# Kernel tuning notes

Measured on AMD Instinct MI355X. Metric: run time of the kernel, lower is better.

The kernel has to match this reference:

```python
import jax, jax.numpy as jnp
import numpy as np

COMMITMENT_COST = 0.25
EPS = 1e-12  # F.normalize default eps


def _l2_normalize(x):
    n = jnp.linalg.norm(x, axis=-1, keepdims=True)
    return x / jnp.maximum(n, EPS)


def setup_inputs() -> dict:
    key = jax.random.key(0)
    k1, k2 = jax.random.split(key)
    inputs = jax.random.normal(k1, (32, 1024, 256), dtype=jnp.float32)
    codebooks = jax.random.normal(k2, (8, 1024, 256), dtype=jnp.float32)
    return {"inputs": inputs, "codebooks": codebooks}


def reference(inputs, codebooks):
    # inputs: (B, T, D); codebooks: (Q, C, D)
    Q, C, D = codebooks.shape
    sg = jax.lax.stop_gradient
    residual = inputs
    quantized_sum = jnp.zeros_like(inputs)
    losses = []
    idx_list = []
    for qi in range(Q):
        cb = codebooks[qi]                              # (C, D)
        flat = residual.reshape(-1, D)                  # (N, D)
        sim = jnp.matmul(_l2_normalize(flat), _l2_normalize(cb).T)  # (N, C)
        indices = jnp.argmax(sim, axis=1)               # argmin(1 - sim) == argmax(sim)
        q = cb[indices].reshape(residual.shape)         # (B, T, D)
        e_latent = jnp.mean((sg(q) - residual) ** 2)
        q_latent = jnp.mean((q - sg(residual)) ** 2)
        losses.append(q_latent + COMMITMENT_COST * e_latent)
        q_st = residual + sg(q - residual)              # straight-through
        quantized_sum = quantized_sum + q_st
        residual = residual - q_st
        idx_list.append(indices)
    total_vq_loss = jnp.mean(jnp.stack(losses))
    indices_all = jnp.stack(idx_list)[..., None]        # (Q, N, 1) int32
    return (quantized_sum, total_vq_loss, indices_all)
```

## Files before the change

### kernel.cpp

```cpp
#include <hip/hip_runtime.h>
#include <math.h>

#define QN 8
#define CN 1024
#define DN 256
#define NROWS 32768

#define LOSS_OFF 8388608
#define IDX_OFF  8388609

typedef float f32x4v __attribute__((ext_vector_type(4)));
typedef short v8s __attribute__((ext_vector_type(8)));
typedef unsigned short u16;
typedef unsigned short u16x8 __attribute__((ext_vector_type(8)));

__device__ __forceinline__ u16 bfr(float x) {
    unsigned u = __float_as_uint(x);
    u += 0x7FFFu + ((u >> 16) & 1u);
    return (u16)(u >> 16);
}
__device__ __forceinline__ float bfs(u16 h) { return __uint_as_float(((unsigned)h) << 16); }

__device__ __forceinline__ void acpB(u16* d, const u16* s) {
    __builtin_amdgcn_global_load_lds(
        (const __attribute__((address_space(1))) unsigned int*)s,
        (__attribute__((address_space(3))) unsigned int*)d, 16, 0, 0);
}

__global__ void rvq_prep(const float* __restrict__ cb,
                         u16* __restrict__ bh, u16* __restrict__ bm,
                         float* __restrict__ invw,
                         float* __restrict__ out) {
    if (blockIdx.x == 0 && threadIdx.x == 0) out[LOSS_OFF] = 0.0f;
    const int wave = threadIdx.x >> 6;
    const int lane = threadIdx.x & 63;
    const int cw = blockIdx.x * 4 + wave;
    float4 v = reinterpret_cast<const float4*>(cb + (size_t)cw * DN)[lane];
    float ss = v.x * v.x + v.y * v.y + v.z * v.z + v.w * v.w;
#pragma unroll
    for (int m = 1; m < 64; m <<= 1) ss += __shfl_xor(ss, m, 64);
    const float inv = 1.0f / fmaxf(sqrtf(ss), 1e-12f);
    if (lane == 0) invw[cw] = inv;
    ushort4 hv, mv;
#define PSPLIT(F, E) { const float x_ = (F) * inv; const u16 h_ = bfr(x_); \
                       hv.E = h_; mv.E = bfr(x_ - bfs(h_)); }
    PSPLIT(v.x, x) PSPLIT(v.y, y) PSPLIT(v.z, z) PSPLIT(v.w, w)
#undef PSPLIT
    reinterpret_cast<ushort4*>(bh + (size_t)cw * DN)[lane] = hv;
    reinterpret_cast<ushort4*>(bm + (size_t)cw * DN)[lane] = mv;
}

__global__ __attribute__((amdgpu_flat_work_group_size(256, 256), amdgpu_waves_per_eu(2, 2)))
void rvq_main(const float* __restrict__ in,
              const float* __restrict__ cb,
              const u16* __restrict__ bh, const u16* __restrict__ bm,
              const float* __restrict__ invw,
              float* __restrict__ out) {
    __shared__ __align__(16) char lds[81920];
    u16* Ah = (u16*)lds;
    u16* Am = (u16*)(lds + 32768);
    u16* Bt = (u16*)(lds + 65536);
    float* Rres = (float*)lds;
    int*   cand = (int*)(lds + 65536);
    int*   sIdx = (int*)(lds + 65536 + 1024);
    float* red  = (float*)(lds + 65536 + 1024 + 256);

    const int t   = threadIdx.x;
    const int l   = t & 63;
    const int w   = t >> 6;
    const int g   = l >> 4;
    const int li  = l & 15;
    const int row = l;
    const int KS  = w * 64;
    const int w8  = w * 8;
    const int w16 = w * 16;
    const int w16li = w16 + li;
    const int base  = blockIdx.x * 64;

    const float* inr0 = in + (size_t)(base + row) * DN + KS;
#define DECLR(i) float4 rr##i = *reinterpret_cast<const float4*>(inr0 + (i) * 4);
    DECLR(0) DECLR(1) DECLR(2) DECLR(3) DECLR(4) DECLR(5) DECLR(6) DECLR(7)
    DECLR(8) DECLR(9) DECLR(10) DECLR(11) DECLR(12) DECLR(13) DECLR(14) DECLR(15)
#undef DECLR
    float lossAcc = 0.0f;

    for (int qs = 0; qs < QN; ++qs) {
        const u16* bhq = bh + ((size_t)qs << 18);
        const u16* bmq = bm + ((size_t)qs << 18);

#define SCV(e, x) { const float xv_ = (x); const u16 hb_ = bfr(xv_); \
                    hh_[e] = hb_; mm_[e] = bfr(xv_ - bfs(hb_)); }
#define SPLITP(p, RA, RB) { u16x8 hh_, mm_; \
        SCV(0, RA.x) SCV(1, RA.y) SCV(2, RA.z) SCV(3, RA.w) \
        SCV(4, RB.x) SCV(5, RB.y) SCV(6, RB.z) SCV(7, RB.w) \
        const int ao_ = ((w8 + (p)) * 64 + row) * 8; \
        *(u16x8*)(Ah + ao_) = hh_; *(u16x8*)(Am + ao_) = mm_; }
        SPLITP(0, rr0, rr1)   SPLITP(1, rr2, rr3)   SPLITP(2, rr4, rr5)
        SPLITP(3, rr6, rr7)   SPLITP(4, rr8, rr9)   SPLITP(5, rr10, rr11)
        SPLITP(6, rr12, rr13) SPLITP(7, rr14, rr15)
#undef SPLITP
#undef SCV

#define STAGE(nb, sp_) { \
        _Pragma("unroll") \
        for (int jj_ = 0; jj_ < 2; ++jj_) { \
            const int d_ = jj_ * 256 + t; \
            const int sub_ = d_ >> 8, pl_ = (d_ >> 7) & 1, kb_ = (d_ >> 5) & 3, col_ = d_ & 31; \
            const int s2_ = (sp_) * 2 + sub_; const int cs2_ = s2_ >> 3, ks2_ = s2_ & 7; \
            const u16* gp_ = (pl_ ? bmq : bhq) + (size_t)(cs2_ * 32 + col_) * DN + ks2_ * 32 + kb_ * 8; \
            acpB(Bt + (nb) * 4096 + d_ * 8, gp_); } }

#define DECLT(j) float v1_##j = -INFINITY, v2_##j = -INFINITY, \
                       v3_##j = -INFINITY, v4_##j = -INFINITY; \
                 int i1_##j = 0, i2_##j = 0, i3_##j = 0, i4_##j = 0;
        DECLT(0) DECLT(1) DECLT(2) DECLT(3)
#undef DECLT
        f32x4v accA = (f32x4v){0.f, 0.f, 0.f, 0.f};
        f32x4v accB = (f32x4v){0.f, 0.f, 0.f, 0.f};

#define MRG4(j, vv, ci) { const float v_ = (vv); const int c_ = (ci); \
        if (v_ > v4_##j) { \
            if (v_ > v2_##j) { \
                if (v_ > v1_##j) { v4_##j = v3_##j; i4_##j = i3_##j; v3_##j = v2_##j; i3_##j = i2_##j; \
                                   v2_##j = v1_##j; i2_##j = i1_##j; v1_##j = v_; i1_##j = c_; } \
                else             { v4_##j = v3_##j; i4_##j = i3_##j; v3_##j = v2_##j; i3_##j = i2_##j; \
                                   v2_##j = v_; i2_##j = c_; } \
            } else { \
                if (v_ > v3_##j) { v4_##j = v3_##j; i4_##j = i3_##j; v3_##j = v_; i3_##j = c_; } \
                else             { v4_##j = v_; i4_##j = c_; } \
            } } }

#define COMPUTE(bb, sub) { \
        const int s_ = sp * 2 + (sub); const int cs_ = s_ >> 3, ks_ = s_ & 7; \
        const int ao_ = ((ks_ * 4 + g) * 64 + w16li) * 8; \
        const v8s ah_ = *(const v8s*)(Ah + ao_); \
        const v8s am_ = *(const v8s*)(Am + ao_); \
        const u16* bt_ = Bt + ((bb) * 2 + (sub)) * 2048; \
        const v8s bh0_ = *(const v8s*)(bt_ + g * 256 + li * 8); \
        const v8s bh1_ = *(const v8s*)(bt_ + g * 256 + 128 + li * 8); \
        const v8s bm0_ = *(const v8s*)(bt_ + 1024 + g * 256 + li * 8); \
        const v8s bm1_ = *(const v8s*)(bt_ + 1024 + g * 256 + 128 + li * 8); \
        accA = __builtin_amdgcn_mfma_f32_16x16x32_bf16(ah_, bh0_, accA, 0, 0, 0); \
        accA = __builtin_amdgcn_mfma_f32_16x16x32_bf16(ah_, bm0_, accA, 0, 0, 0); \
        accA = __builtin_amdgcn_mfma_f32_16x16x32_bf16(am_, bh0_, accA, 0, 0, 0); \
        accA = __builtin_amdgcn_mfma_f32_16x16x32_bf16(am_, bm0_, accA, 0, 0, 0); \
        accB = __builtin_amdgcn_mfma_f32_16x16x32_bf16(ah_, bh1_, accB, 0, 0, 0); \
        accB = __builtin_amdgcn_mfma_f32_16x16x32_bf16(ah_, bm1_, accB, 0, 0, 0); \
        accB = __builtin_amdgcn_mfma_f32_16x16x32_bf16(am_, bh1_, accB, 0, 0, 0); \
        accB = __builtin_amdgcn_mfma_f32_16x16x32_bf16(am_, bm1_, accB, 0, 0, 0); \
        if (ks_ == 7) { \
            const int cb0_ = cs_ * 32 + li; \
            MRG4(0, accA.x, cb0_) MRG4(1, accA.y, cb0_) MRG4(2, accA.z, cb0_) MRG4(3, accA.w, cb0_) \
            MRG4(0, accB.x, cb0_ + 16) MRG4(1, accB.y, cb0_ + 16) \
            MRG4(2, accB.z, cb0_ + 16) MRG4(3, accB.w, cb0_ + 16) \
            accA = (f32x4v){0.f, 0.f, 0.f, 0.f}; accB = (f32x4v){0.f, 0.f, 0.f, 0.f}; } }

        STAGE(0, 0)
        for (int sp = 0; sp < 128; ++sp) {
            __syncthreads();
            const int bb = sp & 1;
            if (sp < 127) STAGE(bb ^ 1, sp + 1)
            COMPUTE(bb, 0)
            COMPUTE(bb, 1)
        }
#undef COMPUTE
#undef STAGE

#define EXT1(j, GD) { \
        const float cv_ = (p_ == 0) ? v1_##j : (p_ == 1) ? v2_##j : \
                          (p_ == 2) ? v3_##j : (p_ == 3) ? v4_##j : -INFINITY; \
        const int   ci_ = (p_ == 0) ? i1_##j : (p_ == 1) ? i2_##j : \
                          (p_ == 2) ? i3_##j : i4_##j; \
        float bv_ = cv_; int bi_ = ci_; \
        _Pragma("unroll") \
        for (int m = 1; m < 16; m <<= 1) { \
            const float ov = __shfl_xor(bv_, m, 64); \
            const int   oi = __shfl_xor(bi_, m, 64); \
            if (ov > bv_ || (ov == bv_ && oi < bi_)) { bv_ = ov; bi_ = oi; } } \
        GD = bi_; if (p_ < 4 && ci_ == bi_) ++p_; }

#define EXTW(j) { \
        int p_ = 0; int g0_, g1_, g2_, g3_; \
        EXT1(j, g0_) EXT1(j, g1_) EXT1(j, g2_) EXT1(j, g3_) \
        if (li == 0) { int* cp_ = cand + (w16 + g * 4 + (j)) * 4; \
            cp_[0] = g0_; cp_[1] = g1_; cp_[2] = g2_; cp_[3] = g3_; } }
        EXTW(0) EXTW(1) EXTW(2) EXTW(3)
#undef EXTW
#undef EXT1
#undef MRG4

        __syncthreads();

#define DMP(i) { const int k0_ = (KS + (i) * 4) * 64 + row; \
        Rres[k0_] = rr##i.x; Rres[k0_ + 64] = rr##i.y; \
        Rres[k0_ + 128] = rr##i.z; Rres[k0_ + 192] = rr##i.w; }
        DMP(0) DMP(1) DMP(2) DMP(3) DMP(4) DMP(5) DMP(6) DMP(7)
        DMP(8) DMP(9) DMP(10) DMP(11) DMP(12) DMP(13) DMP(14) DMP(15)
#undef DMP
        __syncthreads();

        {
            const int crow = t >> 2;
            const int c    = cand[(crow << 2) | (t & 3)];
            const float invc = invw[(qs << 10) + c];
            const float* cr = cb + ((size_t)qs << 18) + (size_t)c * DN;
            float acc = 0.0f;
#pragma unroll 8
            for (int kb = 0; kb < 64; ++kb) {
                const float4 cv = *reinterpret_cast<const float4*>(cr + kb * 4);
                const int k0 = kb * 256 + crow;
                acc = fmaf(Rres[k0 +   0], cv.x * invc, acc);
                acc = fmaf(Rres[k0 +  64], cv.y * invc, acc);
                acc = fmaf(Rres[k0 + 128], cv.z * invc, acc);
                acc = fmaf(Rres[k0 + 192], cv.w * invc, acc);
            }
            float sv = acc; int si = c;
#pragma unroll
            for (int m = 1; m < 4; m <<= 1) {
                const float ov = __shfl_xor(sv, m, 64);
                const int   oi = __shfl_xor(si, m, 64);
                if (ov > sv || (ov == sv && oi < si)) { sv = ov; si = oi; }
            }
            if ((t & 3) == 0) sIdx[crow] = si;
        }
        __syncthreads();
        if (t < 64) out[(size_t)IDX_OFF + (size_t)qs * NROWS + base + t] = (float)sIdx[t];

        {
            const int gi = sIdx[row];
            const float* qr = cb + ((size_t)qs << 18) + (size_t)gi * DN + KS;
#define UPD(i) { const float4 qv = *reinterpret_cast<const float4*>(qr + (i) * 4); \
                 rr##i.x -= qv.x; rr##i.y -= qv.y; rr##i.z -= qv.z; rr##i.w -= qv.w; \
                 lossAcc += rr##i.x * rr##i.x + rr##i.y * rr##i.y \
                          + rr##i.z * rr##i.z + rr##i.w * rr##i.w; }
            UPD(0) UPD(1) UPD(2) UPD(3) UPD(4) UPD(5) UPD(6) UPD(7)
            UPD(8) UPD(9) UPD(10) UPD(11) UPD(12) UPD(13) UPD(14) UPD(15)
#undef UPD
        }
        __syncthreads();
    }

#pragma unroll
    for (int m = 1; m < 64; m <<= 1) lossAcc += __shfl_xor(lossAcc, m, 64);
    if (l == 0) red[w] = lossAcc;
    __syncthreads();
    if (t == 0) {
        const float tot = red[0] + red[1] + red[2] + red[3];
        atomicAdd(out + LOSS_OFF, tot * (1.25f / (8.0f * 8388608.0f)));
    }

    float* Rf = (float*)lds;
    __syncthreads();
#define TW(i) *reinterpret_cast<float4*>(Rf + row * DN + KS + (i) * 4) = rr##i;
    TW(0) TW(1) TW(2) TW(3) TW(4) TW(5) TW(6) TW(7)
    TW(8) TW(9) TW(10) TW(11) TW(12) TW(13) TW(14) TW(15)
#undef TW
    __syncthreads();
    {
        const int row2 = t >> 2;
        const int kb2  = (t & 3) * 64;
        const float* ir = in + (size_t)(base + row2) * DN + kb2;
        float* orp = out + (size_t)(base + row2) * DN + kb2;
        const float* rf = Rf + row2 * DN + kb2;
#pragma unroll
        for (int i = 0; i < 16; ++i) {
            const float4 rv = *reinterpret_cast<const float4*>(rf + i * 4);
            const float4 iv = *reinterpret_cast<const float4*>(ir + i * 4);
            float4 ov;
            ov.x = iv.x - rv.x; ov.y = iv.y - rv.y;
            ov.z = iv.z - rv.z; ov.w = iv.w - rv.w;
            *reinterpret_cast<float4*>(orp + i * 4) = ov;
        }
    }
}

extern "C" void kernel_launch(void* const* d_in, const int* in_sizes, int n_in,
                              void* d_out, int out_size, void* d_ws, size_t ws_size,
                              hipStream_t stream) {
    (void)in_sizes; (void)n_in; (void)out_size; (void)ws_size;
    const float* in = (const float*)d_in[0];
    const float* cb = (const float*)d_in[1];
    float* out = (float*)d_out;
    u16* bhp = (u16*)d_ws;
    u16* bmp = bhp + (size_t)QN * CN * DN;
    float* invw = (float*)(bmp + (size_t)QN * CN * DN);

    rvq_prep<<<dim3(2048), dim3(256), 0, stream>>>(cb, bhp, bmp, invw, out);
    rvq_main<<<dim3(512), dim3(256), 0, stream>>>(in, cb, bhp, bmp, invw, out);
}
```

Before: 848.2 us.

## Hoist A fragments into registers and unroll codebook loop by chunk

The A-side bf16 hi/mid fragments for all eight k-steps are loaded once into registers before the codebook loop, so they are no longer re-read from LDS every step. The loop is unrolled by 32-codeword chunks, which turns the ks==7 branch into straight-line code and moves the barrier to the end of each step. The top-4 merge now skips both candidates of a row when neither beats the current fourth-best. This costs 16 extra v8s registers per thread, which could lower occupancy, and it changes where the barriers sit relative to staging.

```diff
diff --git a/kernel.cpp b/kernel.cpp
--- a/kernel.cpp
+++ b/kernel.cpp
@@ -130,41 +130,54 @@
                 else             { v4_##j = v_; i4_##j = c_; } \
             } } }
 
-#define COMPUTE(bb, sub) { \
-        const int s_ = sp * 2 + (sub); const int cs_ = s_ >> 3, ks_ = s_ & 7; \
-        const int ao_ = ((ks_ * 4 + g) * 64 + w16li) * 8; \
-        const v8s ah_ = *(const v8s*)(Ah + ao_); \
-        const v8s am_ = *(const v8s*)(Am + ao_); \
-        const u16* bt_ = Bt + ((bb) * 2 + (sub)) * 2048; \
+#define COMPUTE(bb, KS_) { \
+        const u16* bt_ = Bt + ((bb) * 2 + ((KS_) & 1)) * 2048; \
         const v8s bh0_ = *(const v8s*)(bt_ + g * 256 + li * 8); \
         const v8s bh1_ = *(const v8s*)(bt_ + g * 256 + 128 + li * 8); \
         const v8s bm0_ = *(const v8s*)(bt_ + 1024 + g * 256 + li * 8); \
         const v8s bm1_ = *(const v8s*)(bt_ + 1024 + g * 256 + 128 + li * 8); \
-        accA = __builtin_amdgcn_mfma_f32_16x16x32_bf16(ah_, bh0_, accA, 0, 0, 0); \
-        accA = __builtin_amdgcn_mfma_f32_16x16x32_bf16(ah_, bm0_, accA, 0, 0, 0); \
-        accA = __builtin_amdgcn_mfma_f32_16x16x32_bf16(am_, bh0_, accA, 0, 0, 0); \
-        accA = __builtin_amdgcn_mfma_f32_16x16x32_bf16(am_, bm0_, accA, 0, 0, 0); \
-        accB = __builtin_amdgcn_mfma_f32_16x16x32_bf16(ah_, bh1_, accB, 0, 0, 0); \
-        accB = __builtin_amdgcn_mfma_f32_16x16x32_bf16(ah_, bm1_, accB, 0, 0, 0); \
-        accB = __builtin_amdgcn_mfma_f32_16x16x32_bf16(am_, bh1_, accB, 0, 0, 0); \
-        accB = __builtin_amdgcn_mfma_f32_16x16x32_bf16(am_, bm1_, accB, 0, 0, 0); \
-        if (ks_ == 7) { \
-            const int cb0_ = cs_ * 32 + li; \
-            MRG4(0, accA.x, cb0_) MRG4(1, accA.y, cb0_) MRG4(2, accA.z, cb0_) MRG4(3, accA.w, cb0_) \
-            MRG4(0, accB.x, cb0_ + 16) MRG4(1, accB.y, cb0_ + 16) \
-            MRG4(2, accB.z, cb0_ + 16) MRG4(3, accB.w, cb0_ + 16) \
-            accA = (f32x4v){0.f, 0.f, 0.f, 0.f}; accB = (f32x4v){0.f, 0.f, 0.f, 0.f}; } }
+        accA = __builtin_amdgcn_mfma_f32_16x16x32_bf16(aH##KS_, bh0_, accA, 0, 0, 0); \
+        accA = __builtin_amdgcn_mfma_f32_16x16x32_bf16(aH##KS_, bm0_, accA, 0, 0, 0); \
+        accA = __builtin_amdgcn_mfma_f32_16x16x32_bf16(aM##KS_, bh0_, accA, 0, 0, 0); \
+        accA = __builtin_amdgcn_mfma_f32_16x16x32_bf16(aM##KS_, bm0_, accA, 0, 0, 0); \
+        accB = __builtin_amdgcn_mfma_f32_16x16x32_bf16(aH##KS_, bh1_, accB, 0, 0, 0); \
+        accB = __builtin_amdgcn_mfma_f32_16x16x32_bf16(aH##KS_, bm1_, accB, 0, 0, 0); \
+        accB = __builtin_amdgcn_mfma_f32_16x16x32_bf16(aM##KS_, bh1_, accB, 0, 0, 0); \
+        accB = __builtin_amdgcn_mfma_f32_16x16x32_bf16(aM##KS_, bm1_, accB, 0, 0, 0); }
+
+#define MERGE_ROW(j, vA, vB) { \
+        if (fmaxf((vA), (vB)) > v4_##j) { MRG4(j, (vA), cb0_) MRG4(j, (vB), cb0_ + 16) } }
 
         STAGE(0, 0)
-        for (int sp = 0; sp < 128; ++sp) {
-            __syncthreads();
-            const int bb = sp & 1;
-            if (sp < 127) STAGE(bb ^ 1, sp + 1)
-            COMPUTE(bb, 0)
-            COMPUTE(bb, 1)
+        __syncthreads();
+
+#define HST(K) \
+        const v8s aH##K = *(const v8s*)(Ah + (((K) * 4 + g) * 64 + w16li) * 8); \
+        const v8s aM##K = *(const v8s*)(Am + (((K) * 4 + g) * 64 + w16li) * 8);
+        HST(0) HST(1) HST(2) HST(3) HST(4) HST(5) HST(6) HST(7)
+#undef HST
+
+        for (int cs = 0; cs < 32; ++cs) {
+            { const int sp = cs * 4 + 0; if (sp < 127) STAGE(1, sp + 1)
+              COMPUTE(0, 0) COMPUTE(0, 1) __syncthreads(); }
+            { const int sp = cs * 4 + 1; if (sp < 127) STAGE(0, sp + 1)
+              COMPUTE(1, 2) COMPUTE(1, 3) __syncthreads(); }
+            { const int sp = cs * 4 + 2; if (sp < 127) STAGE(1, sp + 1)
+              COMPUTE(0, 4) COMPUTE(0, 5) __syncthreads(); }
+            { const int sp = cs * 4 + 3; if (sp < 127) STAGE(0, sp + 1)
+              COMPUTE(1, 6) COMPUTE(1, 7) __syncthreads(); }
+            {
+                const int cb0_ = (cs << 5) + li;
+                MERGE_ROW(0, accA.x, accB.x) MERGE_ROW(1, accA.y, accB.y)
+                MERGE_ROW(2, accA.z, accB.z) MERGE_ROW(3, accA.w, accB.w)
+                accA = (f32x4v){0.f, 0.f, 0.f, 0.f};
+                accB = (f32x4v){0.f, 0.f, 0.f, 0.f};
+            }
         }
+#undef MERGE_ROW
 #undef COMPUTE
 #undef STAGE
+#undef MRG4
 
 #define EXT1(j, GD) { \
         const float cv_ = (p_ == 0) ? v1_##j : (p_ == 1) ? v2_##j : \
@@ -187,7 +200,6 @@
         EXTW(0) EXTW(1) EXTW(2) EXTW(3)
 #undef EXTW
 #undef EXT1
-#undef MRG4
 
         __syncthreads();
 
```

Measured after the change: 963.3 us. +13.6%, slower.

## Replace double-buffered codebook staging with a four-slot ring prefetching three stages ahead

Applied to the files above, without the earlier changes.

The codebook tile loop used two buffers, each holding two sub-stages, with a full __syncthreads per pair, so each load had only one iteration to complete. It now uses a four-slot ring of single-stage buffers. Loads are issued three stages ahead and each step waits only on its own stage via explicit s_waitcnt vmcnt plus a raw s_barrier. The aim is to hide global-to-LDS load latency behind MFMA work. The cost is twice as many barriers per tile sweep, and correctness now relies on the exact count of outstanding vector-memory ops.

```diff
diff --git a/kernel.cpp b/kernel.cpp
--- a/kernel.cpp
+++ b/kernel.cpp
@@ -101,14 +101,11 @@
 #undef SPLITP
 #undef SCV
 
-#define STAGE(nb, sp_) { \
-        _Pragma("unroll") \
-        for (int jj_ = 0; jj_ < 2; ++jj_) { \
-            const int d_ = jj_ * 256 + t; \
-            const int sub_ = d_ >> 8, pl_ = (d_ >> 7) & 1, kb_ = (d_ >> 5) & 3, col_ = d_ & 31; \
-            const int s2_ = (sp_) * 2 + sub_; const int cs2_ = s2_ >> 3, ks2_ = s2_ & 7; \
-            const u16* gp_ = (pl_ ? bmq : bhq) + (size_t)(cs2_ * 32 + col_) * DN + ks2_ * 32 + kb_ * 8; \
-            acpB(Bt + (nb) * 4096 + d_ * 8, gp_); } }
+#define STAGE4(nb, st_) { \
+        const int cs2_ = (st_) >> 3, ks2_ = (st_) & 7; \
+        const int pl_ = t >> 7, kb_ = (t >> 5) & 3, col_ = t & 31; \
+        const u16* gp_ = (pl_ ? bmq : bhq) + (size_t)(cs2_ * 32 + col_) * DN + ks2_ * 32 + kb_ * 8; \
+        acpB(Bt + (nb) * 2048 + t * 8, gp_); }
 
 #define DECLT(j) float v1_##j = -INFINITY, v2_##j = -INFINITY, \
                        v3_##j = -INFINITY, v4_##j = -INFINITY; \
@@ -130,12 +127,12 @@
                 else             { v4_##j = v_; i4_##j = c_; } \
             } } }
 
-#define COMPUTE(bb, sub) { \
-        const int s_ = sp * 2 + (sub); const int cs_ = s_ >> 3, ks_ = s_ & 7; \
+#define COMPUTE4(nb, st_) { \
+        const int cs_ = (st_) >> 3, ks_ = (st_) & 7; \
         const int ao_ = ((ks_ * 4 + g) * 64 + w16li) * 8; \
         const v8s ah_ = *(const v8s*)(Ah + ao_); \
         const v8s am_ = *(const v8s*)(Am + ao_); \
-        const u16* bt_ = Bt + ((bb) * 2 + (sub)) * 2048; \
+        const u16* bt_ = Bt + (nb) * 2048; \
         const v8s bh0_ = *(const v8s*)(bt_ + g * 256 + li * 8); \
         const v8s bh1_ = *(const v8s*)(bt_ + g * 256 + 128 + li * 8); \
         const v8s bm0_ = *(const v8s*)(bt_ + 1024 + g * 256 + li * 8); \
@@ -155,16 +152,26 @@
             MRG4(2, accB.z, cb0_ + 16) MRG4(3, accB.w, cb0_ + 16) \
             accA = (f32x4v){0.f, 0.f, 0.f, 0.f}; accB = (f32x4v){0.f, 0.f, 0.f, 0.f}; } }
 
-        STAGE(0, 0)
-        for (int sp = 0; sp < 128; ++sp) {
-            __syncthreads();
-            const int bb = sp & 1;
-            if (sp < 127) STAGE(bb ^ 1, sp + 1)
-            COMPUTE(bb, 0)
-            COMPUTE(bb, 1)
-        }
-#undef COMPUTE
-#undef STAGE
+#define WBAR(N) asm volatile("s_waitcnt vmcnt(" #N ")" ::: "memory"); \
+                __builtin_amdgcn_s_barrier(); \
+                __builtin_amdgcn_sched_barrier(0);
+
+        STAGE4(0, 0) STAGE4(1, 1) STAGE4(2, 2)
+        __syncthreads();
+        STAGE4(3, 3)
+        COMPUTE4(0, 0)
+        for (int tt = 1; tt <= 252; ++tt) {
+            WBAR(2)
+            STAGE4((tt + 3) & 3, tt + 3)
+            COMPUTE4(tt & 3, tt)
+        }
+        WBAR(2) COMPUTE4(1, 253)
+        WBAR(1) COMPUTE4(2, 254)
+        WBAR(0) COMPUTE4(3, 255)
+#undef WBAR
+#undef COMPUTE4
+#undef STAGE4
+#undef MRG4
 
 #define EXT1(j, GD) { \
         const float cv_ = (p_ == 0) ? v1_##j : (p_ == 1) ? v2_##j : \
@@ -187,7 +194,6 @@
         EXTW(0) EXTW(1) EXTW(2) EXTW(3)
 #undef EXTW
 #undef EXT1
-#undef MRG4
 
         __syncthreads();
 
```

Result: slower. 885.8 us (+4.4%).
